# Kernel tuning notes

Measured on AMD Instinct MI355X. Metric: run time of the kernel, lower is better.

Reference implementation:

```python
import jax, jax.numpy as jnp
import numpy as np

VOCAB, EMBED, HID = 50257, 512, 512
B, SRC = 128, 128


def setup_inputs() -> dict:
    key = jax.random.key(0)
    ks = jax.random.split(key, 16)
    s = 0.02
    emb_tab = jax.random.normal(ks[0], (VOCAB, EMBED), jnp.float32) * s
    emb_tab = emb_tab.at[0].set(0.0)  # padding_idx=0
    return {
        "x": jax.random.randint(ks[1], (B,), 0, VOCAB),
        "decoder_hidden": jax.random.normal(ks[2], (1, B, HID), jnp.float32),
        "source_lens": jax.random.randint(ks[3], (B,), 1, SRC + 1),
        "encoder_outputs": jax.random.normal(ks[4], (B, SRC, HID), jnp.float32),
        "context_vec": jax.random.normal(ks[5], (B, HID), jnp.float32),
        "embedding": emb_tab,
        "w_ih": jax.random.normal(ks[6], (3 * HID, HID + EMBED), jnp.float32) * s,
        "w_hh": jax.random.normal(ks[7], (3 * HID, HID), jnp.float32) * s,
        "b_ih": jax.random.normal(ks[8], (3 * HID,), jnp.float32) * s,
        "b_hh": jax.random.normal(ks[9], (3 * HID,), jnp.float32) * s,
        "Wa": jax.random.normal(ks[10], (HID, HID), jnp.float32) * s,
        "Wc": jax.random.normal(ks[11], (HID, 2 * HID), jnp.float32) * s,
        "fc1_w": jax.random.normal(ks[12], (VOCAB, HID), jnp.float32) * s,
        "fc1_b": jax.random.normal(ks[13], (VOCAB,), jnp.float32) * s,
    }


def _gru_step(inp, h, w_ih, w_hh, b_ih, b_hh):
    # inp: [B, I], h: [B, H] -> h': [B, H]  (PyTorch GRU gate order: r, z, n)
    gi = inp @ w_ih.T + b_ih
    gh = h @ w_hh.T + b_hh
    i_r, i_z, i_n = jnp.split(gi, 3, axis=1)
    h_r, h_z, h_n = jnp.split(gh, 3, axis=1)
    r = jax.nn.sigmoid(i_r + h_r)
    z = jax.nn.sigmoid(i_z + h_z)
    n = jnp.tanh(i_n + r * h_n)
    return (1.0 - z) * n + z * h


def reference(x, decoder_hidden, source_lens, encoder_outputs, context_vec,
              embedding, w_ih, w_hh, b_ih, b_hh, Wa, Wc, fc1_w, fc1_b):
    # embedding lookup (dropout is identity in eval mode)
    emb = embedding[x]                                    # [B, E]
    rnn_in = jnp.concatenate([emb, context_vec], axis=1)  # [B, E+H]
    h = _gru_step(rnn_in, decoder_hidden[0], w_ih, w_hh, b_ih, b_hh)  # [B, H]
    hidden = h[None]                                      # [1, B, H]

    # Luong-style attention (scores laid out [src_len, B] as in original)
    q = h @ Wa.T                                          # [B, H]
    attn_scores = jnp.einsum('bsh,bh->sb', encoder_outputs, q)  # [S, B]
    seq_range = jnp.arange(encoder_outputs.shape[1])      # [S]
    enc_mask = (seq_range[None, :] < source_lens[:, None]).T    # [S, B]
    masked = enc_mask.astype(attn_scores.dtype) * attn_scores
    masked = jnp.where(masked == 0, jnp.asarray(-1e10, masked.dtype), masked)
    a = jax.nn.softmax(masked, axis=0)                    # [S, B]
    ctx = jnp.einsum('sb,bsh->bh', a, encoder_outputs)    # [B, H]
    ctx = jnp.tanh(jnp.concatenate([ctx, h], axis=1) @ Wc.T)    # [B, H]

    logits = ctx @ fc1_w.T + fc1_b                        # [B, V]
    log_probs = jax.nn.log_softmax(logits, axis=1)
    return log_probs, hidden, a, ctx
```

## Files before the change

### kernel.cpp

```cpp
#include <hip/hip_runtime.h>

#define VOCAB 50257
#define EMBED 512
#define HID   512
#define B     128
#define SRC   128
#define NT393 393

typedef __attribute__((ext_vector_type(8))) short short8;
typedef __attribute__((ext_vector_type(4))) float f32x4;

__device__ __forceinline__ unsigned f2bf(float x) {
    unsigned u = __builtin_bit_cast(unsigned, x);
    return (u + 0x7fffu + ((u >> 16) & 1u)) >> 16;
}
__device__ __forceinline__ unsigned pk2(float lo, float hi) {
    return f2bf(lo) | (f2bf(hi) << 16);
}
__device__ __forceinline__ uint4 pk8(const float* p) {
    uint4 r;
    r.x = pk2(p[0], p[1]); r.y = pk2(p[2], p[3]);
    r.z = pk2(p[4], p[5]); r.w = pk2(p[6], p[7]);
    return r;
}
__device__ __forceinline__ uint4 pk8v(float4 a, float4 b) {
    uint4 r;
    r.x = pk2(a.x, a.y); r.y = pk2(a.z, a.w);
    r.z = pk2(b.x, b.y); r.w = pk2(b.z, b.w);
    return r;
}
__device__ __forceinline__ void gll16(const void* g, void* l) {
    __builtin_amdgcn_global_load_lds(
        (const __attribute__((address_space(1))) void*)g,
        (__attribute__((address_space(3))) void*)l, 16, 0, 0);
}


__global__ void k_embed_pack(const int* __restrict__ x, const float* __restrict__ ctxv,
                             const float* __restrict__ emb, const float* __restrict__ h0,
                             uint4* __restrict__ apk_rnn, uint4* __restrict__ apk_h0) {
    __shared__ float buf[1024];
    __shared__ float hbuf[512];
    const int b = blockIdx.x, t = threadIdx.x;
    const int row = x[b];
    if (t < 128) {
        ((float4*)buf)[t]  = ((const float4*)(emb + (size_t)row * EMBED))[t];
        ((float4*)hbuf)[t] = ((const float4*)(h0 + (size_t)b * HID))[t];
    } else {
        ((float4*)buf)[t] = ((const float4*)(ctxv + (size_t)b * HID))[t - 128];
    }
    __syncthreads();
    const int mt = b >> 4, lb = b & 15;
    if (t < 128) {
        int kc = t >> 4, ksl = (t >> 2) & 3, kg = t & 3;
        apk_rnn[((kc * 8 + mt) * 4 + ksl) * 64 + kg * 16 + lb] = pk8(&buf[t * 8]);
    } else if (t < 192) {
        int i = t - 128;
        int kc = i >> 4, ksl = (i >> 2) & 3, kg = i & 3;
        apk_h0[((kc * 8 + mt) * 4 + ksl) * 64 + kg * 16 + lb] = pk8(&hbuf[i * 8]);
    }
}

template <int N, int K, int ACT, int HASB, int PACK>
__global__ __launch_bounds__(256, 2) void k_gemm_ks(
        const uint4* __restrict__ apk, const float* __restrict__ W,
        const float* __restrict__ bias, float* __restrict__ C,
        uint4* __restrict__ apk_out) {
    __shared__ float red[4][128][16];
    const int tid = threadIdx.x, lane = tid & 63, wv = tid >> 6;
    const int n0 = blockIdx.x * 16;
    const int ncol = n0 + (lane & 15);
    const int nc = ncol < N ? ncol : N - 1;
    const int kg = lane >> 4;
    constexpr int SPW = K / 128;
    f32x4 acc[8];
#pragma unroll
    for (int mt = 0; mt < 8; ++mt) acc[mt] = (f32x4)0.f;
    const float4* W4 = (const float4*)W;
    const size_t wb = (size_t)nc * (K / 4) + kg * 2;
#pragma unroll
    for (int s = 0; s < SPW; ++s) {
        const int ks = wv * SPW + s;
        float4 w0 = W4[wb + ks * 8];
        float4 w1 = W4[wb + ks * 8 + 1];
        short8 bf = __builtin_bit_cast(short8, pk8v(w0, w1));
        const uint4* ap = apk + (((ks >> 2) * 8) * 4 + (ks & 3)) * 64 + lane;
#pragma unroll
        for (int mt = 0; mt < 8; ++mt) {
            short8 af = __builtin_bit_cast(short8, ap[mt * 256]);
            acc[mt] = __builtin_amdgcn_mfma_f32_16x16x32_bf16(af, bf, acc[mt], 0, 0, 0);
        }
    }
#pragma unroll
    for (int mt = 0; mt < 8; ++mt)
#pragma unroll
        for (int j = 0; j < 4; ++j)
            red[wv][mt * 16 + kg * 4 + j][lane & 15] = acc[mt][j];
    __syncthreads();
#pragma unroll
    for (int i = 0; i < 8; ++i) {
        int o = tid + i * 256;
        int r = o >> 4, c = o & 15;
        float v = red[0][r][c] + red[1][r][c] + red[2][r][c] + red[3][r][c];
        if (HASB) v += bias[n0 + c];
        if (ACT) v = tanhf(v);
        C[(size_t)r * N + n0 + c] = v;
        if (PACK) red[0][r][c] = v;
    }
    if constexpr (PACK) {
        __syncthreads();
        int r = tid >> 1, hf = tid & 1;
        float tmp[8];
#pragma unroll
        for (int z = 0; z < 8; ++z) tmp[z] = red[0][r][hf * 8 + z];
        int k0 = n0 + hf * 8;
        int kc = k0 >> 7, ksl = (k0 >> 5) & 3, kg2 = (k0 >> 3) & 3;
        apk_out[((kc * 8 + (r >> 4)) * 4 + ksl) * 64 + kg2 * 16 + (r & 15)] = pk8(tmp);
    }
}

__global__ void k_gru(const float* __restrict__ gi, const float* __restrict__ gh,
                      const float* __restrict__ h0, float* __restrict__ h,
                      uint4* __restrict__ apk_h) {
    __shared__ float hsh[256];
    const int t = threadIdx.x;
    const int idx = blockIdx.x * 256 + t;
    const int b = blockIdx.x >> 1, half = blockIdx.x & 1;
    const int j = half * 256 + t;
    const float* gib = gi + (size_t)b * 1536;
    const float* ghb = gh + (size_t)b * 1536;
    float ir = gib[j], iz = gib[512 + j], inn = gib[1024 + j];
    float hr = ghb[j], hz = ghb[512 + j], hn = ghb[1024 + j];
    float r = 1.f / (1.f + expf(-(ir + hr)));
    float z = 1.f / (1.f + expf(-(iz + hz)));
    float nn = tanhf(inn + r * hn);
    float hv = (1.f - z) * nn + z * h0[idx];
    h[idx] = hv;
    hsh[t] = hv;
    __syncthreads();
    if (t < 32) {
        int k0 = half * 256 + t * 8;
        int kc = k0 >> 7, ksl = (k0 >> 5) & 3, kg = (k0 >> 3) & 3;
        apk_h[((kc * 8 + (b >> 4)) * 4 + ksl) * 64 + kg * 16 + (b & 15)] = pk8(&hsh[t * 8]);
    }
}

__global__ __launch_bounds__(512) void k_attn(const float* __restrict__ enc,
        const float* __restrict__ q, const int* __restrict__ lens,
        const float* __restrict__ h, float* __restrict__ a_out,
        uint4* __restrict__ apk_cat) {
    __shared__ float qs[512];
    __shared__ float red[128];
    __shared__ float aw[128];
    __shared__ float catsh[1024];
    const int b = blockIdx.x, t = threadIdx.x;
    qs[t] = q[(size_t)b * 512 + t];
    __syncthreads();
    const int srow = t >> 2, part = t & 3;
    const float* ep = enc + ((size_t)b * SRC + srow) * 512 + part * 128;
    float s = 0.f;
#pragma unroll
    for (int k4 = 0; k4 < 32; ++k4) {
        float4 e = ((const float4*)ep)[k4];
        float4 qq = *(const float4*)&qs[part * 128 + k4 * 4];
        s = fmaf(e.x, qq.x, fmaf(e.y, qq.y, fmaf(e.z, qq.z, fmaf(e.w, qq.w, s))));
    }
    s += __shfl_xor(s, 1);
    s += __shfl_xor(s, 2);
    if (part == 0) {
        int len = lens[b];
        float val = (srow < len) ? s : 0.f;
        if (val == 0.f) val = -1e10f;
        red[srow] = val;
        aw[srow] = val;
    }
    __syncthreads();
    for (int off = 64; off > 0; off >>= 1) {
        if (t < off) red[t] = fmaxf(red[t], red[t + off]);
        __syncthreads();
    }
    float mx = red[0];
    __syncthreads();
    if (t < 128) { float e = expf(aw[t] - mx); aw[t] = e; red[t] = e; }
    __syncthreads();
    for (int off = 64; off > 0; off >>= 1) {
        if (t < off) red[t] += red[t + off];
        __syncthreads();
    }
    float denom = red[0];
    if (t < 128) {
        float av = aw[t] / denom;
        aw[t] = av;
        a_out[(size_t)t * B + b] = av;
    }
    __syncthreads();
    float a0 = 0.f;
    const float* e2 = enc + (size_t)b * (SRC * 512) + t;
#pragma unroll 4
    for (int s2 = 0; s2 < SRC; ++s2) a0 = fmaf(aw[s2], e2[(size_t)s2 * 512], a0);
    catsh[t] = a0;
    catsh[512 + t] = h[(size_t)b * 512 + t];
    __syncthreads();
    if (t < 128) {
        int kc = t >> 4, ksl = (t >> 2) & 3, kg = t & 3;
        apk_cat[((kc * 8 + (b >> 4)) * 4 + ksl) * 64 + kg * 16 + (b & 15)] =
            pk8(&catsh[t * 8]);
    }
}

__global__ __launch_bounds__(512, 2) void k_fc1p(
        const uint4* __restrict__ apk, const float* __restrict__ W,
        const float* __restrict__ bias, float* __restrict__ C,
        float2* __restrict__ pout) {
    __shared__ uint4 As[8192];
    __shared__ float pm8[8][128], ps8[8][128];
    const int tid = threadIdx.x, lane = tid & 63, wv = tid >> 6;
    const int kg = lane >> 4;
#pragma unroll
    for (int it = 0; it < 16; ++it)
        gll16(apk + it * 512 + tid, As + it * 512 + tid);
    __syncthreads();
    const float4* W4 = (const float4*)W;

    for (int nt = blockIdx.x; nt < NT393; nt += 256) {
        const int ncol = nt * 128 + wv * 16 + (lane & 15);
        const bool valid = ncol < VOCAB;
        const int nc = valid ? ncol : VOCAB - 1;
        const size_t wb = (size_t)nc * 128 + kg * 2;
        f32x4 acc[8];
#pragma unroll
        for (int mt = 0; mt < 8; ++mt) acc[mt] = (f32x4)0.f;
        float4 wr[32];
#pragma unroll
        for (int i = 0; i < 16; ++i) {
            wr[2 * i]     = W4[wb + (size_t)i * 8];
            wr[2 * i + 1] = W4[wb + (size_t)i * 8 + 1];
        }
#pragma unroll
        for (int ks = 0; ks < 16; ++ks) {
            short8 bf = __builtin_bit_cast(short8, pk8v(wr[2 * ks], wr[2 * ks + 1]));
            const int base = ((ks >> 2) * 32 + (ks & 3)) * 64 + lane;
#pragma unroll
            for (int mt = 0; mt < 8; ++mt) {
                short8 af = __builtin_bit_cast(short8, As[base + mt * 256]);
                acc[mt] = __builtin_amdgcn_mfma_f32_16x16x32_bf16(af, bf, acc[mt], 0, 0, 0);
            }
        }
        float bb = bias[nc];
#pragma unroll
        for (int mt = 0; mt < 8; ++mt) {
#pragma unroll
            for (int j = 0; j < 4; ++j) {
                float v = acc[mt][j] + bb;
                int row = mt * 16 + kg * 4 + j;
                if (valid) C[(size_t)row * VOCAB + ncol] = v;
                float val = valid ? v : -1e30f;
                float m16 = val;
                m16 = fmaxf(m16, __shfl_xor(m16, 1));
                m16 = fmaxf(m16, __shfl_xor(m16, 2));
                m16 = fmaxf(m16, __shfl_xor(m16, 4));
                m16 = fmaxf(m16, __shfl_xor(m16, 8));
                float e = valid ? __expf(val - m16) : 0.f;
                e += __shfl_xor(e, 1);
                e += __shfl_xor(e, 2);
                e += __shfl_xor(e, 4);
                e += __shfl_xor(e, 8);
                if ((lane & 15) == 0) { pm8[wv][row] = m16; ps8[wv][row] = e; }
            }
        }
        __syncthreads();
        if (tid < 128) {
            float m = pm8[0][tid], s = ps8[0][tid];
#pragma unroll
            for (int w = 1; w < 8; ++w) {
                float m2 = pm8[w][tid], s2 = ps8[w][tid];
                float mm = fmaxf(m, m2);
                s = s * __expf(m - mm) + s2 * __expf(m2 - mm);
                m = mm;
            }
            pout[(size_t)tid * NT393 + nt] = make_float2(m, s);
        }
        __syncthreads();
    }
}

__global__ __launch_bounds__(256) void k_lse_final(const float2* __restrict__ pout,
                                                   float* __restrict__ L, int nblk) {
    const int row = blockIdx.x, t = threadIdx.x;
    float m = -1e30f, s = 0.f;
    for (int i = t; i < nblk; i += 256) {
        float2 p = pout[(size_t)row * nblk + i];
        float mm = fmaxf(m, p.x);
        s = s * __expf(m - mm) + p.y * __expf(p.x - mm);
        m = mm;
    }
    __shared__ float sm[256], ss[256];
    sm[t] = m; ss[t] = s; __syncthreads();
    for (int off = 128; off > 0; off >>= 1) {
        if (t < off) {
            float m2 = sm[t + off], s2 = ss[t + off];
            float mm = fmaxf(sm[t], m2);
            ss[t] = ss[t] * __expf(sm[t] - mm) + s2 * __expf(m2 - mm);
            sm[t] = mm;
        }
        __syncthreads();
    }
    if (t == 0) L[row] = sm[0] + logf(ss[0]);
}

__global__ __launch_bounds__(512) void k_lsub(float* __restrict__ logits,
                                              const float* __restrict__ L) {
    const int b = blockIdx.y;
    const float l = L[b];
    float* row = logits + (size_t)b * VOCAB;
    int c0 = (blockIdx.x * 512 + threadIdx.x) * 4;
    if (c0 + 4 <= VOCAB) {
        float4 x = *(float4*)(row + c0);
        x.x -= l; x.y -= l; x.z -= l; x.w -= l;
        *(float4*)(row + c0) = x;
    } else {
        for (int c = c0; c < VOCAB; ++c) row[c] -= l;
    }
}

__global__ __launch_bounds__(1024) void k_lse_sub(float* __restrict__ logits) {
    const int b = blockIdx.x, t = threadIdx.x;
    float* row = logits + (size_t)b * VOCAB;
    const int N4 = VOCAB >> 2;
    float m = -1e30f, s = 0.f;
    for (int i = t; i < N4; i += 1024) {
        float4 x = ((const float4*)row)[i];
        float xs[4] = {x.x, x.y, x.z, x.w};
#pragma unroll
        for (int j = 0; j < 4; ++j) {
            float v = xs[j];
            if (v > m) { s = s * __expf(m - v) + 1.f; m = v; }
            else        s += __expf(v - m);
        }
    }
    if (t == 0) {
        float v = row[VOCAB - 1];
        if (v > m) { s = s * __expf(m - v) + 1.f; m = v; }
        else        s += __expf(v - m);
    }
    __shared__ float sm[1024], ss[1024];
    sm[t] = m; ss[t] = s;
    __syncthreads();
    for (int off = 512; off > 0; off >>= 1) {
        if (t < off) {
            float m2 = sm[t + off], s2 = ss[t + off];
            float mm = fmaxf(sm[t], m2);
            ss[t] = ss[t] * __expf(sm[t] - mm) + s2 * __expf(m2 - mm);
            sm[t] = mm;
        }
        __syncthreads();
    }
    __shared__ float Lsh;
    if (t == 0) Lsh = sm[0] + logf(ss[0]);
    __syncthreads();
    float L = Lsh;
    for (int i = t; i < N4; i += 1024) {
        float4 x = ((const float4*)row)[i];
        x.x -= L; x.y -= L; x.z -= L; x.w -= L;
        ((float4*)row)[i] = x;
    }
    if (t == 0) row[VOCAB - 1] -= L;
}

extern "C" void kernel_launch(void* const* d_in, const int* in_sizes, int n_in,
                              void* d_out, int out_size, void* d_ws, size_t ws_size,
                              hipStream_t stream) {
    const int*   x    = (const int*)d_in[0];
    const float* h0   = (const float*)d_in[1];
    const int*   lens = (const int*)d_in[2];
    const float* enc  = (const float*)d_in[3];
    const float* ctxv = (const float*)d_in[4];
    const float* emb  = (const float*)d_in[5];
    const float* wih  = (const float*)d_in[6];
    const float* whh  = (const float*)d_in[7];
    const float* bih  = (const float*)d_in[8];
    const float* bhh  = (const float*)d_in[9];
    const float* Wa   = (const float*)d_in[10];
    const float* Wc   = (const float*)d_in[11];
    const float* fc1w = (const float*)d_in[12];
    const float* fc1b = (const float*)d_in[13];

    float* out     = (float*)d_out;
    float* outLogp = out;
    float* outHid  = out + (size_t)B * VOCAB;
    float* outA    = outHid + (size_t)B * HID;
    float* outCtx  = outA + (size_t)SRC * B;

    float* gi = outLogp;
    float* gh = gi + B * 1536;
    float* q  = gh + B * 1536;
    uint4* apk_rnn = (uint4*)(q + B * HID);
    uint4* apk_h0  = apk_rnn + 16384;
    uint4* apk_h   = apk_h0 + 8192;
    uint4* apk_cat = apk_h + 8192;

    uint4*  apk_ctx = (uint4*)d_ws;
    size_t  off_pout = 131072;
    size_t  off_L    = off_pout + (size_t)B * NT393 * sizeof(float2);
    bool bigws = ws_size >= off_L + 512;
    float2* pout = bigws ? (float2*)((char*)d_ws + off_pout) : nullptr;
    float*  Lb   = bigws ? (float*)((char*)d_ws + off_L) : nullptr;

    k_embed_pack<<<dim3(B), dim3(256), 0, stream>>>(x, ctxv, emb, h0, apk_rnn, apk_h0);
    k_gemm_ks<1536, 1024, 0, 1, 0><<<dim3(96), dim3(256), 0, stream>>>(
        apk_rnn, wih, bih, gi, nullptr);
    k_gemm_ks<1536, 512, 0, 1, 0><<<dim3(96), dim3(256), 0, stream>>>(
        apk_h0, whh, bhh, gh, nullptr);
    k_gru<<<dim3(256), dim3(256), 0, stream>>>(gi, gh, h0, outHid, apk_h);
    k_gemm_ks<512, 512, 0, 0, 0><<<dim3(32), dim3(256), 0, stream>>>(
        apk_h, Wa, nullptr, q, nullptr);
    k_attn<<<dim3(B), dim3(512), 0, stream>>>(enc, q, lens, outHid, outA, apk_cat);
    k_gemm_ks<512, 1024, 1, 0, 1><<<dim3(32), dim3(256), 0, stream>>>(
        apk_cat, Wc, nullptr, outCtx, apk_ctx);
    if (bigws) {
        k_fc1p<<<dim3(256), dim3(512), 0, stream>>>(apk_ctx, fc1w, fc1b, outLogp, pout);
        k_lse_final<<<dim3(B), dim3(256), 0, stream>>>(pout, Lb, NT393);
        k_lsub<<<dim3(25, B), dim3(512), 0, stream>>>(outLogp, Lb);
    } else {
        k_fc1p<<<dim3(256), dim3(512), 0, stream>>>(apk_ctx, fc1w, fc1b, outLogp, nullptr);
        k_lse_sub<<<dim3(B), dim3(1024), 0, stream>>>(outLogp);
    }
}
```

Baseline: 122.7 us.

## Software-pipeline fc1 weight loads in chunks and double-buffer softmax partials

Splits the fc1 GEMM's per-tile weight load into four register chunks that alternate between two buffers. Each chunk's global load is issued while the previous chunk feeds the MFMAs, and the first chunk of the next tile is prefetched during the last chunk of the current one. The partial max/sum shared buffer is double-buffered, which drops the trailing __syncthreads per tile, and the partial-LSE path can now be skipped when pout is null. This aims to hide global-load latency behind matrix math and cut register pressure, but gives up the single large batch of loads that was in flight at once.

Result: no change. 123.8 us (+0.9%).

```diff
diff --git a/kernel.cpp b/kernel.cpp
--- a/kernel.cpp
+++ b/kernel.cpp
@@ -208,12 +208,30 @@
     }
 }
 
+#define FC1_LOADC(dst, wbase, c)                                        \
+    _Pragma("unroll")                                                   \
+    for (int q = 0; q < 4; ++q) {                                       \
+        dst[2 * q]     = W4[(wbase) + (size_t)((4 * (c) + q) * 8)];     \
+        dst[2 * q + 1] = W4[(wbase) + (size_t)((4 * (c) + q) * 8 + 1)]; \
+    }
+#define FC1_CONS(src, c)                                                \
+    _Pragma("unroll")                                                   \
+    for (int q = 0; q < 4; ++q) {                                       \
+        short8 bf = __builtin_bit_cast(short8, pk8v(src[2 * q], src[2 * q + 1])); \
+        const int base = ((c) * 32 + q) * 64 + lane;                    \
+        _Pragma("unroll")                                               \
+        for (int mt = 0; mt < 8; ++mt) {                                \
+            short8 af = __builtin_bit_cast(short8, As[base + mt * 256]);\
+            acc[mt] = __builtin_amdgcn_mfma_f32_16x16x32_bf16(af, bf, acc[mt], 0, 0, 0); \
+        }                                                               \
+    }
+
 __global__ __launch_bounds__(512, 2) void k_fc1p(
         const uint4* __restrict__ apk, const float* __restrict__ W,
         const float* __restrict__ bias, float* __restrict__ C,
         float2* __restrict__ pout) {
     __shared__ uint4 As[8192];
-    __shared__ float pm8[8][128], ps8[8][128];
+    __shared__ float2 pms[2][8][128];
     const int tid = threadIdx.x, lane = tid & 63, wv = tid >> 6;
     const int kg = lane >> 4;
 #pragma unroll
@@ -222,30 +240,38 @@
     __syncthreads();
     const float4* W4 = (const float4*)W;
 
-    for (int nt = blockIdx.x; nt < NT393; nt += 256) {
+    float4 Ab[8], Bb[8];
+    int nt0 = blockIdx.x;
+    {
+        int ncol0 = nt0 * 128 + wv * 16 + (lane & 15);
+        size_t wb0 = (size_t)(ncol0 < VOCAB ? ncol0 : VOCAB - 1) * 128 + kg * 2;
+        FC1_LOADC(Ab, wb0, 0);
+    }
+    int pb = 0;
+    size_t wb;
+    {
+        int ncol0 = nt0 * 128 + wv * 16 + (lane & 15);
+        wb = (size_t)(ncol0 < VOCAB ? ncol0 : VOCAB - 1) * 128 + kg * 2;
+    }
+    for (int nt = nt0; nt < NT393; nt += 256) {
         const int ncol = nt * 128 + wv * 16 + (lane & 15);
         const bool valid = ncol < VOCAB;
         const int nc = valid ? ncol : VOCAB - 1;
-        const size_t wb = (size_t)nc * 128 + kg * 2;
+        const int ntn = (nt + 256 < NT393) ? nt + 256 : NT393 - 1;
+        const int ncoln = ntn * 128 + wv * 16 + (lane & 15);
+        const size_t wbn = (size_t)(ncoln < VOCAB ? ncoln : VOCAB - 1) * 128 + kg * 2;
         f32x4 acc[8];
 #pragma unroll
         for (int mt = 0; mt < 8; ++mt) acc[mt] = (f32x4)0.f;
-        float4 wr[32];
-#pragma unroll
-        for (int i = 0; i < 16; ++i) {
-            wr[2 * i]     = W4[wb + (size_t)i * 8];
-            wr[2 * i + 1] = W4[wb + (size_t)i * 8 + 1];
-        }
-#pragma unroll
-        for (int ks = 0; ks < 16; ++ks) {
-            short8 bf = __builtin_bit_cast(short8, pk8v(wr[2 * ks], wr[2 * ks + 1]));
-            const int base = ((ks >> 2) * 32 + (ks & 3)) * 64 + lane;
-#pragma unroll
-            for (int mt = 0; mt < 8; ++mt) {
-                short8 af = __builtin_bit_cast(short8, As[base + mt * 256]);
-                acc[mt] = __builtin_amdgcn_mfma_f32_16x16x32_bf16(af, bf, acc[mt], 0, 0, 0);
-            }
-        }
+        FC1_LOADC(Bb, wb, 1);
+        FC1_CONS(Ab, 0);
+        FC1_LOADC(Ab, wb, 2);
+        FC1_CONS(Bb, 1);
+        FC1_LOADC(Bb, wb, 3);
+        FC1_CONS(Ab, 2);
+        FC1_LOADC(Ab, wbn, 0);
+        FC1_CONS(Bb, 3);
+
         float bb = bias[nc];
 #pragma unroll
         for (int mt = 0; mt < 8; ++mt) {
@@ -254,33 +280,39 @@
                 float v = acc[mt][j] + bb;
                 int row = mt * 16 + kg * 4 + j;
                 if (valid) C[(size_t)row * VOCAB + ncol] = v;
-                float val = valid ? v : -1e30f;
-                float m16 = val;
-                m16 = fmaxf(m16, __shfl_xor(m16, 1));
-                m16 = fmaxf(m16, __shfl_xor(m16, 2));
-                m16 = fmaxf(m16, __shfl_xor(m16, 4));
-                m16 = fmaxf(m16, __shfl_xor(m16, 8));
-                float e = valid ? __expf(val - m16) : 0.f;
-                e += __shfl_xor(e, 1);
-                e += __shfl_xor(e, 2);
-                e += __shfl_xor(e, 4);
-                e += __shfl_xor(e, 8);
-                if ((lane & 15) == 0) { pm8[wv][row] = m16; ps8[wv][row] = e; }
+                if (pout) {
+                    float val = valid ? v : -1e30f;
+                    float m16 = val;
+                    m16 = fmaxf(m16, __shfl_xor(m16, 1));
+                    m16 = fmaxf(m16, __shfl_xor(m16, 2));
+                    m16 = fmaxf(m16, __shfl_xor(m16, 4));
+                    m16 = fmaxf(m16, __shfl_xor(m16, 8));
+                    float e = valid ? __expf(val - m16) : 0.f;
+                    e += __shfl_xor(e, 1);
+                    e += __shfl_xor(e, 2);
+                    e += __shfl_xor(e, 4);
+                    e += __shfl_xor(e, 8);
+                    if ((lane & 15) == 0) pms[pb][wv][row] = make_float2(m16, e);
+                }
             }
         }
-        __syncthreads();
-        if (tid < 128) {
-            float m = pm8[0][tid], s = ps8[0][tid];
-#pragma unroll
-            for (int w = 1; w < 8; ++w) {
-                float m2 = pm8[w][tid], s2 = ps8[w][tid];
-                float mm = fmaxf(m, m2);
-                s = s * __expf(m - mm) + s2 * __expf(m2 - mm);
-                m = mm;
+        if (pout) {
+            __syncthreads();
+            if (tid < 128) {
+                float2 p = pms[pb][0][tid];
+                float m = p.x, s = p.y;
+#pragma unroll
+                for (int w = 1; w < 8; ++w) {
+                    float2 p2 = pms[pb][w][tid];
+                    float mm = fmaxf(m, p2.x);
+                    s = s * __expf(m - mm) + p2.y * __expf(p2.x - mm);
+                    m = mm;
+                }
+                pout[(size_t)tid * NT393 + nt] = make_float2(m, s);
             }
-            pout[(size_t)tid * NT393 + nt] = make_float2(m, s);
-        }
-        __syncthreads();
+            pb ^= 1;
+        }
+        wb = wbn;
     }
 }
 
```

## Split fc1 into single-wave blocks and merge GRU input/hidden GEMMs into one launch

Applied to the files above, without the earlier changes.

The fc1 vocabulary projection moves from 256 persistent 512-thread blocks, which staged the packed activations in LDS, to 1571 single-wave blocks. Each of these computes 32 vocab columns, reads activation fragments straight from global memory, and writes per-block partial log-sum-exp values. The two GRU gate GEMMs (input and hidden) are fused into one 192-block launch that branches on block index. The goal is more parallelism across the large weight stream and fewer kernel launches. The cost is more redundant global reads of the activations, plus a larger partial array for the final LSE reduction.

After: 136.2 us. +11.0%, slower.

```diff
diff --git a/kernel.cpp b/kernel.cpp
--- a/kernel.cpp
+++ b/kernel.cpp
@@ -5,7 +5,7 @@
 #define HID   512
 #define B     128
 #define SRC   128
-#define NT393 393
+#define FBLK  1571
 
 typedef __attribute__((ext_vector_type(8))) short short8;
 typedef __attribute__((ext_vector_type(4))) float f32x4;
@@ -28,11 +28,6 @@
     r.x = pk2(a.x, a.y); r.y = pk2(a.z, a.w);
     r.z = pk2(b.x, b.y); r.w = pk2(b.z, b.w);
     return r;
-}
-__device__ __forceinline__ void gll16(const void* g, void* l) {
-    __builtin_amdgcn_global_load_lds(
-        (const __attribute__((address_space(1))) void*)g,
-        (__attribute__((address_space(3))) void*)l, 16, 0, 0);
 }
 
 
@@ -58,6 +53,59 @@
         int i = t - 128;
         int kc = i >> 4, ksl = (i >> 2) & 3, kg = i & 3;
         apk_h0[((kc * 8 + mt) * 4 + ksl) * 64 + kg * 16 + lb] = pk8(&hbuf[i * 8]);
+    }
+}
+
+__global__ __launch_bounds__(256, 2) void k_gemm2(
+        const uint4* __restrict__ apkA, const float* __restrict__ WA,
+        const float* __restrict__ bA, float* __restrict__ CA, int KA,
+        const uint4* __restrict__ apkB, const float* __restrict__ WB,
+        const float* __restrict__ bB, float* __restrict__ CB, int KB,
+        int nblkA) {
+    const bool isB = (int)blockIdx.x >= nblkA;
+    const uint4* apk = isB ? apkB : apkA;
+    const float* W   = isB ? WB : WA;
+    const float* bias= isB ? bB : bA;
+    float* C         = isB ? CB : CA;
+    const int K      = isB ? KB : KA;
+    const int bid    = isB ? (int)blockIdx.x - nblkA : (int)blockIdx.x;
+    const int N = 1536;
+    __shared__ float red[4][128][16];
+    const int tid = threadIdx.x, lane = tid & 63, wv = tid >> 6;
+    const int n0 = bid * 16;
+    const int ncol = n0 + (lane & 15);
+    const int kg = lane >> 4;
+    const int spw = K >> 7;
+    f32x4 acc[8];
+#pragma unroll
+    for (int mt = 0; mt < 8; ++mt) acc[mt] = (f32x4)0.f;
+    const float4* W4 = (const float4*)W;
+    const size_t wb = (size_t)ncol * (K >> 2) + kg * 2;
+    for (int s = 0; s < spw; ++s) {
+        const int ks = wv * spw + s;
+        float4 w0 = W4[wb + ks * 8];
+        float4 w1 = W4[wb + ks * 8 + 1];
+        short8 bf = __builtin_bit_cast(short8, pk8v(w0, w1));
+        const uint4* ap = apk + ((size_t)(ks >> 2) * 32 + (ks & 3)) * 64 + lane;
+#pragma unroll
+        for (int mt = 0; mt < 8; ++mt) {
+            short8 af = __builtin_bit_cast(short8, ap[mt * 256]);
+            acc[mt] = __builtin_amdgcn_mfma_f32_16x16x32_bf16(af, bf, acc[mt], 0, 0, 0);
+        }
+    }
+#pragma unroll
+    for (int mt = 0; mt < 8; ++mt)
+#pragma unroll
+        for (int j = 0; j < 4; ++j)
+            red[wv][mt * 16 + kg * 4 + j][lane & 15] = acc[mt][j];
+    __syncthreads();
+#pragma unroll
+    for (int i = 0; i < 8; ++i) {
+        int o = tid + i * 256;
+        int r = o >> 4, c = o & 15;
+        float v = red[0][r][c] + red[1][r][c] + red[2][r][c] + red[3][r][c];
+        v += bias[n0 + c];
+        C[(size_t)r * N + n0 + c] = v;
     }
 }
 
@@ -208,79 +256,66 @@
     }
 }
 
-__global__ __launch_bounds__(512, 2) void k_fc1p(
+__global__ __launch_bounds__(64) void k_fc1d(
         const uint4* __restrict__ apk, const float* __restrict__ W,
         const float* __restrict__ bias, float* __restrict__ C,
-        float2* __restrict__ pout) {
-    __shared__ uint4 As[8192];
-    __shared__ float pm8[8][128], ps8[8][128];
-    const int tid = threadIdx.x, lane = tid & 63, wv = tid >> 6;
+        float2* __restrict__ pout, int nblk) {
+    const int lane = threadIdx.x;
     const int kg = lane >> 4;
-#pragma unroll
-    for (int it = 0; it < 16; ++it)
-        gll16(apk + it * 512 + tid, As + it * 512 + tid);
-    __syncthreads();
+    const int c0 = blockIdx.x * 32 + (lane & 15);
+    const int c1 = c0 + 16;
+    const int nc0 = c0 < VOCAB ? c0 : VOCAB - 1;
+    const int nc1 = c1 < VOCAB ? c1 : VOCAB - 1;
     const float4* W4 = (const float4*)W;
-
-    for (int nt = blockIdx.x; nt < NT393; nt += 256) {
-        const int ncol = nt * 128 + wv * 16 + (lane & 15);
-        const bool valid = ncol < VOCAB;
-        const int nc = valid ? ncol : VOCAB - 1;
-        const size_t wb = (size_t)nc * 128 + kg * 2;
-        f32x4 acc[8];
-#pragma unroll
-        for (int mt = 0; mt < 8; ++mt) acc[mt] = (f32x4)0.f;
-        float4 wr[32];
-#pragma unroll
-        for (int i = 0; i < 16; ++i) {
-            wr[2 * i]     = W4[wb + (size_t)i * 8];
-            wr[2 * i + 1] = W4[wb + (size_t)i * 8 + 1];
-        }
-#pragma unroll
-        for (int ks = 0; ks < 16; ++ks) {
-            short8 bf = __builtin_bit_cast(short8, pk8v(wr[2 * ks], wr[2 * ks + 1]));
-            const int base = ((ks >> 2) * 32 + (ks & 3)) * 64 + lane;
-#pragma unroll
-            for (int mt = 0; mt < 8; ++mt) {
-                short8 af = __builtin_bit_cast(short8, As[base + mt * 256]);
-                acc[mt] = __builtin_amdgcn_mfma_f32_16x16x32_bf16(af, bf, acc[mt], 0, 0, 0);
-            }
-        }
-        float bb = bias[nc];
+    const size_t wb0 = (size_t)nc0 * 128 + kg * 2;
+    const size_t wb1 = (size_t)nc1 * 128 + kg * 2;
+    f32x4 acc0[8], acc1[8];
+#pragma unroll
+    for (int mt = 0; mt < 8; ++mt) { acc0[mt] = (f32x4)0.f; acc1[mt] = (f32x4)0.f; }
+#pragma unroll
+    for (int ks = 0; ks < 16; ++ks) {
+        float4 wa0 = W4[wb0 + ks * 8];
+        float4 wa1 = W4[wb0 + ks * 8 + 1];
+        float4 wc0 = W4[wb1 + ks * 8];
+        float4 wc1 = W4[wb1 + ks * 8 + 1];
+        short8 bf0 = __builtin_bit_cast(short8, pk8v(wa0, wa1));
+        short8 bf1 = __builtin_bit_cast(short8, pk8v(wc0, wc1));
+        const uint4* ap = apk + ((size_t)(ks >> 2) * 32 + (ks & 3)) * 64 + lane;
 #pragma unroll
         for (int mt = 0; mt < 8; ++mt) {
-#pragma unroll
-            for (int j = 0; j < 4; ++j) {
-                float v = acc[mt][j] + bb;
-                int row = mt * 16 + kg * 4 + j;
-                if (valid) C[(size_t)row * VOCAB + ncol] = v;
-                float val = valid ? v : -1e30f;
-                float m16 = val;
-                m16 = fmaxf(m16, __shfl_xor(m16, 1));
-                m16 = fmaxf(m16, __shfl_xor(m16, 2));
-                m16 = fmaxf(m16, __shfl_xor(m16, 4));
-                m16 = fmaxf(m16, __shfl_xor(m16, 8));
-                float e = valid ? __expf(val - m16) : 0.f;
+            short8 af = __builtin_bit_cast(short8, ap[mt * 256]);
+            acc0[mt] = __builtin_amdgcn_mfma_f32_16x16x32_bf16(af, bf0, acc0[mt], 0, 0, 0);
+            acc1[mt] = __builtin_amdgcn_mfma_f32_16x16x32_bf16(af, bf1, acc1[mt], 0, 0, 0);
+        }
+    }
+    const float bb0 = bias[nc0], bb1 = bias[nc1];
+#pragma unroll
+    for (int mt = 0; mt < 8; ++mt) {
+#pragma unroll
+        for (int j = 0; j < 4; ++j) {
+            const int row = mt * 16 + kg * 4 + j;
+            float v0 = acc0[mt][j] + bb0;
+            float v1 = acc1[mt][j] + bb1;
+            if (c0 < VOCAB) C[(size_t)row * VOCAB + c0] = v0;
+            if (c1 < VOCAB) C[(size_t)row * VOCAB + c1] = v1;
+            if (pout) {
+                float va = c0 < VOCAB ? v0 : -1e30f;
+                float vb = c1 < VOCAB ? v1 : -1e30f;
+                float m = fmaxf(va, vb);
+                m = fmaxf(m, __shfl_xor(m, 1));
+                m = fmaxf(m, __shfl_xor(m, 2));
+                m = fmaxf(m, __shfl_xor(m, 4));
+                m = fmaxf(m, __shfl_xor(m, 8));
+                float e = (c0 < VOCAB ? __expf(va - m) : 0.f)
+                        + (c1 < VOCAB ? __expf(vb - m) : 0.f);
                 e += __shfl_xor(e, 1);
                 e += __shfl_xor(e, 2);
                 e += __shfl_xor(e, 4);
                 e += __shfl_xor(e, 8);
-                if ((lane & 15) == 0) { pm8[wv][row] = m16; ps8[wv][row] = e; }
+                if ((lane & 15) == 0)
+                    pout[(size_t)row * nblk + blockIdx.x] = make_float2(m, e);
             }
         }
-        __syncthreads();
-        if (tid < 128) {
-            float m = pm8[0][tid], s = ps8[0][tid];
-#pragma unroll
-            for (int w = 1; w < 8; ++w) {
-                float m2 = pm8[w][tid], s2 = ps8[w][tid];
-                float mm = fmaxf(m, m2);
-                s = s * __expf(m - mm) + s2 * __expf(m2 - mm);
-                m = mm;
-            }
-            pout[(size_t)tid * NT393 + nt] = make_float2(m, s);
-        }
-        __syncthreads();
     }
 }
 
@@ -401,28 +436,27 @@
 
     uint4*  apk_ctx = (uint4*)d_ws;
     size_t  off_pout = 131072;
-    size_t  off_L    = off_pout + (size_t)B * NT393 * sizeof(float2);
+    size_t  off_L    = off_pout + (size_t)B * FBLK * sizeof(float2);
     bool bigws = ws_size >= off_L + 512;
     float2* pout = bigws ? (float2*)((char*)d_ws + off_pout) : nullptr;
     float*  Lb   = bigws ? (float*)((char*)d_ws + off_L) : nullptr;
 
     k_embed_pack<<<dim3(B), dim3(256), 0, stream>>>(x, ctxv, emb, h0, apk_rnn, apk_h0);
-    k_gemm_ks<1536, 1024, 0, 1, 0><<<dim3(96), dim3(256), 0, stream>>>(
-        apk_rnn, wih, bih, gi, nullptr);
-    k_gemm_ks<1536, 512, 0, 1, 0><<<dim3(96), dim3(256), 0, stream>>>(
-        apk_h0, whh, bhh, gh, nullptr);
+    k_gemm2<<<dim3(192), dim3(256), 0, stream>>>(
+        apk_rnn, wih, bih, gi, 1024,
+        apk_h0, whh, bhh, gh, 512, 96);
     k_gru<<<dim3(256), dim3(256), 0, stream>>>(gi, gh, h0, outHid, apk_h);
     k_gemm_ks<512, 512, 0, 0, 0><<<dim3(32), dim3(256), 0, stream>>>(
         apk_h, Wa, nullptr, q, nullptr);
     k_attn<<<dim3(B), dim3(512), 0, stream>>>(enc, q, lens, outHid, outA, apk_cat);
     k_gemm_ks<512, 1024, 1, 0, 1><<<dim3(32), dim3(256), 0, stream>>>(
         apk_cat, Wc, nullptr, outCtx, apk_ctx);
+    k_fc1d<<<dim3(FBLK), dim3(64), 0, stream>>>(apk_ctx, fc1w, fc1b, outLogp,
+                                                pout, FBLK);
     if (bigws) {
-        k_fc1p<<<dim3(256), dim3(512), 0, stream>>>(apk_ctx, fc1w, fc1b, outLogp, pout);
-        k_lse_final<<<dim3(B), dim3(256), 0, stream>>>(pout, Lb, NT393);
+        k_lse_final<<<dim3(B), dim3(256), 0, stream>>>(pout, Lb, FBLK);
         k_lsub<<<dim3(25, B), dim3(512), 0, stream>>>(outLogp, Lb);
     } else {
-        k_fc1p<<<dim3(256), dim3(512), 0, stream>>>(apk_ctx, fc1w, fc1b, outLogp, nullptr);
         k_lse_sub<<<dim3(B), dim3(1024), 0, stream>>>(outLogp);
     }
 }
```
